# Optimization experiments

Measured on AMD Instinct MI355X. Metric: run time of the kernel, lower is better.

## Reference

```python
import jax, jax.numpy as jnp
import numpy as np

B, T, S, D, V = 32, 2048, 256, 1024, 56
STAR_PENALTY = -1.0
NEG = -1e30  # -inf surrogate that is safe for gradients


def setup_inputs() -> dict:
    key = jax.random.key(0)
    k1, k2, k3 = jax.random.split(key, 3)
    features = jax.random.normal(k1, (B, T, D), jnp.float32)
    targets = jax.random.randint(k2, (B, S), 1, V)  # 0 is the blank; labels in [1, V)
    W = jax.random.normal(k3, (V, D), jnp.float32) * (1.0 / 32.0)  # 1/sqrt(D)
    b = jnp.zeros((V,), jnp.float32)
    input_lengths = jnp.full((B,), T, jnp.int32)
    target_lengths = jnp.full((B,), S, jnp.int32)
    return dict(features=features, W=W, b=b, targets=targets,
                input_lengths=input_lengths, target_lengths=target_lengths)


def _star_ctc_losses(logp, targets, input_lengths, target_lengths, star_penalty):
    """Star-CTC forward (DP) score.
    logp: (T, N, C) log-softmax emissions; targets: (N, S) labels (blank=0 excluded).
    Extended state sequence [*, t1, *, t2, ..., tS, *]: star states play the role of
    CTC blanks but act as penalized wildcards, emitting logsumexp(logp)+star_penalty
    (== star_penalty for normalized log-probs). Standard CTC transition topology:
    self-loop, advance by 1, advance by 2 into a token state when it differs from the
    previous token. Returns per-sequence negative log-likelihood, shape (N,)."""
    Tlen, N, C = logp.shape
    Slen = targets.shape[1]
    L = 2 * Slen + 1
    ext = jnp.zeros((N, L), targets.dtype).at[:, 1::2].set(targets)  # (N, L)
    is_star = (jnp.arange(L) % 2 == 0)[None, :]                      # (1, L)
    prev2 = jnp.pad(ext[:, :-2], ((0, 0), (2, 0)), constant_values=-1)
    allow_skip = (~is_star) & (ext != prev2)                         # (N, L)

    def emit(logp_t):  # logp_t: (N, C) -> (N, L)
        star_e = star_penalty + jax.nn.logsumexp(logp_t, axis=-1, keepdims=True)
        tok_e = jnp.take_along_axis(logp_t, ext, axis=-1)
        return jnp.where(is_star, star_e, tok_e)

    alpha0 = jnp.where(jnp.arange(L)[None, :] < 2, emit(logp[0]), NEG)

    def step(alpha, xs):
        logp_t, t = xs
        a1 = jnp.pad(alpha[:, :-1], ((0, 0), (1, 0)), constant_values=NEG)
        a2 = jnp.where(allow_skip,
                       jnp.pad(alpha[:, :-2], ((0, 0), (2, 0)), constant_values=NEG),
                       NEG)
        new = jnp.logaddexp(jnp.logaddexp(alpha, a1), a2) + emit(logp_t)
        new = jnp.where(t < input_lengths[:, None], new, alpha)  # freeze past input_length
        return new, None

    alpha, _ = jax.lax.scan(step, alpha0, (logp[1:], jnp.arange(1, Tlen)))
    last = 2 * target_lengths                  # index of the final star state
    rows = jnp.arange(N)
    score = jnp.logaddexp(alpha[rows, last], alpha[rows, last - 1])
    return -score


def reference(features, W, b, targets, input_lengths, target_lengths):
    # classifier + log_softmax (Dropout(0.2) is identity at eval time)
    logits = jnp.einsum('btd,vd->btv', features, W) + b
    logp = jax.nn.log_softmax(logits.astype(jnp.float32), axis=-1)
    logp = jnp.transpose(logp, (1, 0, 2))      # (T, N, C) as in logits.permute(1,0,2)
    losses = _star_ctc_losses(logp, targets, input_lengths, target_lengths, STAR_PENALTY)
    # ctc_reduce_mean: length-normalized mean loss
    return jnp.mean(losses / target_lengths.astype(losses.dtype))
```

## Files before the change

### kernel.cpp

```cpp
#include <hip/hip_runtime.h>
#include <hip/hip_bf16.h>
#include <math.h>

typedef __attribute__((ext_vector_type(4))) float f32x4;
typedef __attribute__((ext_vector_type(8))) short s16x8;

#define LOG2E 1.4426950408889634f
#define LN2f  0.6931471805599453f
#define INV_E 0.36787944117144233f

__device__ __forceinline__ short bfc(float x) {
  unsigned u = __float_as_uint(x);
  unsigned r = u + 0x7fffu + ((u >> 16) & 1u);
  return (short)(r >> 16);
}

__device__ __forceinline__ unsigned pk2(float x, float y) {
  union { __hip_bfloat162 h; unsigned u; } c;
  c.h = __float22bfloat162_rn(make_float2(x, y));
  return c.u;
}

__device__ __forceinline__ float bperm(float v, int byte_addr) {
  return __int_as_float(__builtin_amdgcn_ds_bpermute(byte_addr, __float_as_int(v)));
}

__device__ __forceinline__ float rdlane(float v, int lane) {
  return __int_as_float(__builtin_amdgcn_readlane(__float_as_int(v), lane));
}

__global__ void conv_w(const float* __restrict__ W, short* __restrict__ Wb,
                       int V, int D) {
  int idx = blockIdx.x * blockDim.x + threadIdx.x;
  if (idx >= 64 * D) return;
  int row = idx / D, col = idx - row * D;
  Wb[idx] = (row < V) ? bfc(W[(size_t)row * D + col]) : (short)0;
}

__global__ __launch_bounds__(256) void gemm_pexp(
    const float* __restrict__ feat, const short* __restrict__ Wb,
    const float* __restrict__ bias, float* __restrict__ pt,
    int nrows, int D, int V) {
  const int lane = threadIdx.x & 63;
  const int wave = threadIdx.x >> 6;
  const int m_lo = lane & 15;
  const int q = lane >> 4;
  const int rowbase = (blockIdx.x * 4 + wave) * 32;

  int arow0 = rowbase + m_lo;
  int arow1 = rowbase + 16 + m_lo;
  if (arow0 >= nrows) arow0 = nrows - 1;
  if (arow1 >= nrows) arow1 = nrows - 1;
  const float* Ap0 = feat + (size_t)arow0 * D + q * 8;
  const float* Ap1 = feat + (size_t)arow1 * D + q * 8;
  const short* Bp = Wb + (size_t)m_lo * D + q * 8;
  const size_t bstr = (size_t)16 * D;

  f32x4 acc[2][4];
  #pragma unroll
  for (int g = 0; g < 2; ++g)
    #pragma unroll
    for (int ni = 0; ni < 4; ++ni) acc[g][ni] = (f32x4){0.f, 0.f, 0.f, 0.f};

  float4 al0 = *(const float4*)(Ap0);
  float4 ah0 = *(const float4*)(Ap0 + 4);
  float4 al1 = *(const float4*)(Ap1);
  float4 ah1 = *(const float4*)(Ap1 + 4);
  s16x8 b0 = *(const s16x8*)(Bp);
  s16x8 b1 = *(const s16x8*)(Bp + bstr);
  s16x8 b2 = *(const s16x8*)(Bp + 2 * bstr);
  s16x8 b3 = *(const s16x8*)(Bp + 3 * bstr);

  for (int k0 = 0; k0 < D; k0 += 32) {
    const int kn = (k0 + 32 < D) ? (k0 + 32) : 0;
    const float* Ap0n = feat + (size_t)arow0 * D + kn + q * 8;
    const float* Ap1n = feat + (size_t)arow1 * D + kn + q * 8;
    const short* Bpn = Wb + (size_t)m_lo * D + kn + q * 8;
    float4 nal0 = *(const float4*)(Ap0n);
    float4 nah0 = *(const float4*)(Ap0n + 4);
    float4 nal1 = *(const float4*)(Ap1n);
    float4 nah1 = *(const float4*)(Ap1n + 4);
    s16x8 nb0 = *(const s16x8*)(Bpn);
    s16x8 nb1 = *(const s16x8*)(Bpn + bstr);
    s16x8 nb2 = *(const s16x8*)(Bpn + 2 * bstr);
    s16x8 nb3 = *(const s16x8*)(Bpn + 3 * bstr);

    union { s16x8 v; unsigned u[4]; } av0, av1;
    av0.u[0] = pk2(al0.x, al0.y); av0.u[1] = pk2(al0.z, al0.w);
    av0.u[2] = pk2(ah0.x, ah0.y); av0.u[3] = pk2(ah0.z, ah0.w);
    av1.u[0] = pk2(al1.x, al1.y); av1.u[1] = pk2(al1.z, al1.w);
    av1.u[2] = pk2(ah1.x, ah1.y); av1.u[3] = pk2(ah1.z, ah1.w);

    acc[0][0] = __builtin_amdgcn_mfma_f32_16x16x32_bf16(av0.v, b0, acc[0][0], 0, 0, 0);
    acc[0][1] = __builtin_amdgcn_mfma_f32_16x16x32_bf16(av0.v, b1, acc[0][1], 0, 0, 0);
    acc[0][2] = __builtin_amdgcn_mfma_f32_16x16x32_bf16(av0.v, b2, acc[0][2], 0, 0, 0);
    acc[0][3] = __builtin_amdgcn_mfma_f32_16x16x32_bf16(av0.v, b3, acc[0][3], 0, 0, 0);
    acc[1][0] = __builtin_amdgcn_mfma_f32_16x16x32_bf16(av1.v, b0, acc[1][0], 0, 0, 0);
    acc[1][1] = __builtin_amdgcn_mfma_f32_16x16x32_bf16(av1.v, b1, acc[1][1], 0, 0, 0);
    acc[1][2] = __builtin_amdgcn_mfma_f32_16x16x32_bf16(av1.v, b2, acc[1][2], 0, 0, 0);
    acc[1][3] = __builtin_amdgcn_mfma_f32_16x16x32_bf16(av1.v, b3, acc[1][3], 0, 0, 0);

    al0 = nal0; ah0 = nah0; al1 = nal1; ah1 = nah1;
    b0 = nb0; b1 = nb1; b2 = nb2; b3 = nb3;
  }

  float bias_v[4];
  #pragma unroll
  for (int ni = 0; ni < 4; ++ni) {
    int col = ni * 16 + m_lo;
    bias_v[ni] = (col < V) ? bias[col] : 0.f;
  }

  #pragma unroll
  for (int g = 0; g < 2; ++g) {
    #pragma unroll
    for (int r = 0; r < 4; ++r) {
      int grow = rowbase + g * 16 + q * 4 + r;
      float lg[4];
      #pragma unroll
      for (int ni = 0; ni < 4; ++ni) {
        int col = ni * 16 + m_lo;
        lg[ni] = (col < V) ? (acc[g][ni][r] + bias_v[ni]) : -1e30f;
      }
      float m = fmaxf(fmaxf(lg[0], lg[1]), fmaxf(lg[2], lg[3]));
      #pragma unroll
      for (int off = 1; off < 16; off <<= 1) m = fmaxf(m, __shfl_xor(m, off));
      float p[4];
      #pragma unroll
      for (int ni = 0; ni < 4; ++ni) p[ni] = exp2f((lg[ni] - m) * LOG2E);
      float s = (p[0] + p[1]) + (p[2] + p[3]);
      #pragma unroll
      for (int off = 1; off < 16; off <<= 1) s += __shfl_xor(s, off);

      if (grow < nrows) {
        float* orow = pt + (size_t)grow * 64;
        orow[m_lo] = p[0];
        orow[16 + m_lo] = p[1];
        orow[32 + m_lo] = p[2];
        if (m_lo < 8)       orow[48 + m_lo] = p[3];
        else if (m_lo == 8) orow[56] = logf(s);
        else if (m_lo == 9) orow[57] = s * INV_E;
        else                orow[48 + m_lo] = 0.f;
      }
    }
  }
}

__global__ __launch_bounds__(64) void star_dp(
    const float* __restrict__ pt, const int* __restrict__ targets,
    const int* __restrict__ in_len, const int* __restrict__ tgt_len,
    float* __restrict__ partial, int T, int S) {
  const int n = blockIdx.x;
  const int lane = threadIdx.x;
  const float* row = pt + (size_t)n * T * 64;
  const int len = in_len[n];
  const int tl = tgt_len[n];
  const int* tg = targets + (size_t)n * S;

  const int s0 = lane * 4;
  int lab1 = (s0     < S) ? tg[s0]     : 0;
  int lab3 = (s0 + 1 < S) ? tg[s0 + 1] : 0;
  int lab5 = (s0 + 2 < S) ? tg[s0 + 2] : 0;
  int lab7 = (s0 + 3 < S) ? tg[s0 + 3] : 0;
  int labm1 = __shfl_up(lab7, 1);
  int labm3 = __shfl_up(lab5, 1);
  const bool sk1 = (lane > 0) && (lab1 != labm1);
  const bool sk3 = (lab3 != lab1);
  const bool sk5 = (lab5 != lab3);
  const bool sk7 = (lab7 != lab5);
  const bool skm1 = (labm1 != labm3);
  const int ad1 = lab1 << 2, ad3 = lab3 << 2, ad5 = lab5 << 2, ad7 = lab7 << 2;
  const int adm1 = labm1 << 2;

  float a0 = 0, a1 = 0, a2 = 0, a3 = 0, a4 = 0, a5 = 0, a6 = 0, a7 = 0, a8 = 0;
  float m1 = 0.f, m2 = 0.f, m3 = 0.f;
  int eps = 0, eL = 0;
  bool act = (lane == 0);

#define ROWL(t) row[(size_t)(((t) < len) ? (t) : (len - 1)) * 64 + lane]

  float rc = row[lane];
  {
    float star = rdlane(rc, 57);
    float e1i = bperm(rc, ad1);
    if (lane == 0) { a0 = star; a1 = e1i; }
  }
  float ksum = rc;

  float rr0 = ROWL(1), rr1 = ROWL(2), rr2 = ROWL(3), rr3 = ROWL(4);
  float rr4 = ROWL(5), rr5 = ROWL(6), rr6 = ROWL(7), rr7 = ROWL(8);

  float es0v = rdlane(rr0, 57);
  float e1a = bperm(rr0, ad1), e3a = bperm(rr0, ad3);
  float e5a = bperm(rr0, ad5), e7a = bperm(rr0, ad7);
  float em1a = bperm(rr0, adm1);
  float es1v = rdlane(rr1, 57);
  float e1b = bperm(rr1, ad1), e3b = bperm(rr1, ad3);
  float e5b = bperm(rr1, ad5), e7b = bperm(rr1, ad7);

#define RENORM()                                                             \
  do {                                                                       \
    float mx = fmaxf(fmaxf(fmaxf(a0, a1), fmaxf(a2, a3)),                    \
                     fmaxf(fmaxf(a4, a5), fmaxf(a6, a7)));                   \
    mx = fmaxf(mx, a8);                                                      \
    int e = (int)((__float_as_uint(mx) >> 23) & 255) - 126;                  \
    e = (act && mx > 0.f) ? e : 0;                                           \
    a0 = ldexpf(a0, -e); a1 = ldexpf(a1, -e); a2 = ldexpf(a2, -e);           \
    a3 = ldexpf(a3, -e); a4 = ldexpf(a4, -e); a5 = ldexpf(a5, -e);           \
    a6 = ldexpf(a6, -e); a7 = ldexpf(a7, -e); a8 = ldexpf(a8, -e);           \
    eps += e;                                                                \
  } while (0)

#define PAIR(C0, C1, N0, N1, P0, P1, DOREN)                                  \
  do {                                                                       \
    ksum += C0; ksum += C1;                                                  \
    if (!act) eps = eL;                                                      \
    bool inc = (lane != 0) &&                                                \
               ((m1 != 0.f) || (m2 != 0.f) || (m3 != 0.f));                  \
    int d = inc ? (eL - eps) : 0;                                            \
    if (__builtin_expect(d > 24, 0)) {                  \
      a0 = ldexpf(a0, -d); a1 = ldexpf(a1, -d); a2 = ldexpf(a2, -d);         \
      a3 = ldexpf(a3, -d); a4 = ldexpf(a4, -d); a5 = ldexpf(a5, -d);         \
      a6 = ldexpf(a6, -d); a7 = ldexpf(a7, -d); a8 = ldexpf(a8, -d);         \
      eps += d;                                      \
    } else {                                                                 \
      m1 = ldexpf(m1, d); m2 = ldexpf(m2, d); m3 = ldexpf(m3, d);            \
    }                                                                        \
    act = act || (m1 != 0.f) || (m2 != 0.f) || (m3 != 0.f);                  \
                  \
    a8 = (a8 + a7) * es0v;                                                   \
    a7 = (a7 + a6 + (sk7 ? a5 : 0.f)) * e7a;                                 \
    a6 = (a6 + a5) * es0v;                                                   \
    a5 = (a5 + a4 + (sk5 ? a3 : 0.f)) * e5a;                                 \
    a4 = (a4 + a3) * es0v;                                                   \
    a3 = (a3 + a2 + (sk3 ? a1 : 0.f)) * e3a;                                 \
    a2 = (a2 + a1) * es0v;                                                   \
    a1 = (a1 + a0 + (sk1 ? m1 : 0.f)) * e1a;                                 \
    a0 = (a0 + m1) * es0v;                                                   \
    m1 = (m1 + m2 + (skm1 ? m3 : 0.f)) * em1a;                               \
                                                             \
    a8 = (a8 + a7) * es1v;                                                   \
    a7 = (a7 + a6 + (sk7 ? a5 : 0.f)) * e7b;                                 \
    a6 = (a6 + a5) * es1v;                                                   \
    a5 = (a5 + a4 + (sk5 ? a3 : 0.f)) * e5b;                                 \
    a4 = (a4 + a3) * es1v;                                                   \
    a3 = (a3 + a2 + (sk3 ? a1 : 0.f)) * e3b;                                 \
    a2 = (a2 + a1) * es1v;                                                   \
    a1 = (a1 + a0 + (sk1 ? m1 : 0.f)) * e1b;                                 \
    a0 = (a0 + m1) * es1v;                                                   \
    C0 = ROWL(P0); C1 = ROWL(P1);                     \
    if (DOREN) RENORM();                                                     \
      \
    es0v = rdlane(N0, 57);                                                   \
    e1a = bperm(N0, ad1); e3a = bperm(N0, ad3);                              \
    e5a = bperm(N0, ad5); e7a = bperm(N0, ad7);                              \
    em1a = bperm(N0, adm1);                                                  \
    es1v = rdlane(N1, 57);                                                   \
    e1b = bperm(N1, ad1); e3b = bperm(N1, ad3);                              \
    e5b = bperm(N1, ad5); e7b = bperm(N1, ad7);                              \
                          \
    m3 = __shfl_up(a5, 1); m2 = __shfl_up(a6, 1); m1 = __shfl_up(a7, 1);     \
    eL = __shfl_up(eps, 1);                                                  \
    if (lane == 0) { m1 = 0.f; m2 = 0.f; m3 = 0.f; }                         \
  } while (0)

  int t0 = 1;
  for (; t0 + 8 <= len; t0 += 8) {
    PAIR(rr0, rr1, rr2, rr3, t0 + 8,  t0 + 9,  false);
    PAIR(rr2, rr3, rr4, rr5, t0 + 10, t0 + 11, false);
    PAIR(rr4, rr5, rr6, rr7, t0 + 12, t0 + 13, false);
    PAIR(rr6, rr7, rr0, rr1, t0 + 14, t0 + 15, true);
  }

  for (int t = t0; t < len; ++t) {
    float cur = ROWL(t);
    float esv = rdlane(cur, 57);
    float e1v = bperm(cur, ad1), e3v = bperm(cur, ad3);
    float e5v = bperm(cur, ad5), e7v = bperm(cur, ad7);
    ksum += cur;
    if (!act) eps = eL;
    bool inc = (lane != 0) && (m1 != 0.f);
    int d = inc ? (eL - eps) : 0;
    float m1s;
    if (__builtin_expect(d > 24, 0)) {
      a0 = ldexpf(a0, -d); a1 = ldexpf(a1, -d); a2 = ldexpf(a2, -d);
      a3 = ldexpf(a3, -d); a4 = ldexpf(a4, -d); a5 = ldexpf(a5, -d);
      a6 = ldexpf(a6, -d); a7 = ldexpf(a7, -d); a8 = ldexpf(a8, -d);
      eps += d; m1s = m1;
    } else {
      m1s = inc ? ldexpf(m1, d) : 0.f;
    }
    act = act || (m1s != 0.f);
    a8 = (a8 + a7) * esv;
    a7 = (a7 + a6 + (sk7 ? a5 : 0.f)) * e7v;
    a6 = (a6 + a5) * esv;
    a5 = (a5 + a4 + (sk5 ? a3 : 0.f)) * e5v;
    a4 = (a4 + a3) * esv;
    a3 = (a3 + a2 + (sk3 ? a1 : 0.f)) * e3v;
    a2 = (a2 + a1) * esv;
    a1 = (a1 + a0 + (sk1 ? m1s : 0.f)) * e1v;
    a0 = (a0 + m1s) * esv;
    if ((t & 7) == 0) RENORM();
    m1 = __shfl_up(a7, 1);
    eL = __shfl_up(eps, 1);
    if (lane == 0) m1 = 0.f;
  }

  __shared__ float sh[64 * 9];
  __shared__ int she[64];
  sh[lane * 9 + 0] = a0; sh[lane * 9 + 1] = a1; sh[lane * 9 + 2] = a2;
  sh[lane * 9 + 3] = a3; sh[lane * 9 + 4] = a4; sh[lane * 9 + 5] = a5;
  sh[lane * 9 + 6] = a6; sh[lane * 9 + 7] = a7; sh[lane * 9 + 8] = a8;
  she[lane] = eps;
  float k56 = __shfl(ksum, 56);
  __syncthreads();
  if (lane == 0) {
    int last = 2 * tl;
    int kx = last >> 3, jx = last & 7;
    if (kx > 63) { kx = 63; jx = last - 504; }
    int ky = (last - 1) >> 3, jy = (last - 1) & 7;
    float sx = sh[kx * 9 + jx]; int ex = she[kx];
    float sy = sh[ky * 9 + jy]; int ey = she[ky];
    int em = (ex > ey) ? ex : ey;
    float v = ldexpf(sx, ex - em) + ldexpf(sy, ey - em);
    float score = logf(v) + (float)em * LN2f - k56;
    partial[n] = -score / (float)tl;
  }
}

__global__ void reduce_mean(const float* __restrict__ partial,
                            float* __restrict__ out, int B) {
  float v = 0.f;
  for (int i = threadIdx.x; i < B; i += 64) v += partial[i];
  #pragma unroll
  for (int off = 32; off > 0; off >>= 1) v += __shfl_down(v, off, 64);
  if (threadIdx.x == 0) out[0] = v / (float)B;
}

extern "C" void kernel_launch(void* const* d_in, const int* in_sizes, int n_in,
                              void* d_out, int out_size, void* d_ws, size_t ws_size,
                              hipStream_t stream) {
  const float* feat = (const float*)d_in[0];
  const float* W = (const float*)d_in[1];
  const float* bias = (const float*)d_in[2];
  const int* targets = (const int*)d_in[3];
  const int* in_len = (const int*)d_in[4];
  const int* tgt_len = (const int*)d_in[5];
  float* out = (float*)d_out;

  const int V = in_sizes[2];
  const int D = in_sizes[1] / V;
  const int B = in_sizes[4];
  const int T = in_sizes[0] / (B * D);
  const int S = in_sizes[3] / B;
  const int nrows = B * T;

  float* pt = (float*)d_ws;
  float* partial = pt + (size_t)nrows * 64;
  short* Wb = (short*)(partial + B);

  conv_w<<<(64 * D + 255) / 256, 256, 0, stream>>>(W, Wb, V, D);

  dim3 g1((nrows + 127) / 128);
  gemm_pexp<<<g1, 256, 0, stream>>>(feat, Wb, bias, pt, nrows, D, V);

  star_dp<<<B, 64, 0, stream>>>(pt, targets, in_len, tgt_len, partial, T, S);

  reduce_mean<<<1, 64, 0, stream>>>(partial, out, B);
}
```

Measured before the change: 723.1 us.

## Fuse GEMM and star-CTC DP into one kernel with per-chunk ready flags

Merges the emission GEMM/softmax kernel and the sequential DP kernel into one launch. The first B blocks run the DP and spin on per-(batch, 128-timestep chunk) flags set with release atomics by GEMM blocks, so the DP can start before the whole GEMM finishes and the two phases overlap. The final state lookup also moves from shared memory to register selection plus shuffles. The cost is spin-waiting on flags, an extra memset, and a dependence on DP blocks being scheduled early. Since DP blocks have the lowest indices, GEMM blocks can still occupy the GPU alongside them.

Result: slower. 754.8 us (+4.4%).

```diff
diff --git a/kernel.cpp b/kernel.cpp
--- a/kernel.cpp
+++ b/kernel.cpp
@@ -27,6 +27,21 @@
 
 __device__ __forceinline__ float rdlane(float v, int lane) {
   return __int_as_float(__builtin_amdgcn_readlane(__float_as_int(v), lane));
+}
+
+__device__ __forceinline__ float pick9(int j, float a0, float a1, float a2,
+                                       float a3, float a4, float a5, float a6,
+                                       float a7, float a8) {
+  float v = a0;
+  if (j == 1) v = a1;
+  if (j == 2) v = a2;
+  if (j == 3) v = a3;
+  if (j == 4) v = a4;
+  if (j == 5) v = a5;
+  if (j == 6) v = a6;
+  if (j == 7) v = a7;
+  if (j == 8) v = a8;
+  return v;
 }
 
 __global__ void conv_w(const float* __restrict__ W, short* __restrict__ Wb,
@@ -37,125 +52,154 @@
   Wb[idx] = (row < V) ? bfc(W[(size_t)row * D + col]) : (short)0;
 }
 
-__global__ __launch_bounds__(256) void gemm_pexp(
+__global__ __launch_bounds__(256) void fused_gemm_star(
     const float* __restrict__ feat, const short* __restrict__ Wb,
     const float* __restrict__ bias, float* __restrict__ pt,
-    int nrows, int D, int V) {
-  const int lane = threadIdx.x & 63;
-  const int wave = threadIdx.x >> 6;
-  const int m_lo = lane & 15;
-  const int q = lane >> 4;
-  const int rowbase = (blockIdx.x * 4 + wave) * 32;
-
-  int arow0 = rowbase + m_lo;
-  int arow1 = rowbase + 16 + m_lo;
-  if (arow0 >= nrows) arow0 = nrows - 1;
-  if (arow1 >= nrows) arow1 = nrows - 1;
-  const float* Ap0 = feat + (size_t)arow0 * D + q * 8;
-  const float* Ap1 = feat + (size_t)arow1 * D + q * 8;
-  const short* Bp = Wb + (size_t)m_lo * D + q * 8;
-  const size_t bstr = (size_t)16 * D;
-
-  f32x4 acc[2][4];
-  #pragma unroll
-  for (int g = 0; g < 2; ++g)
+    int* __restrict__ flags,
+    const int* __restrict__ targets, const int* __restrict__ in_len,
+    const int* __restrict__ tgt_len, float* __restrict__ partial,
+    int nrows, int D, int V, int T, int S, int B, int CPB) {
+
+  if ((int)blockIdx.x >= B) {
+    const int j = blockIdx.x - B;
+    const int b = j % B;
+    const int c = j / B;
+    const int tc0 = c * 128;
+    const int rlen = (T - tc0 < 128) ? (T - tc0) : 128;
+    const int rowlim = b * T + tc0 + rlen;
+
+    const int lane = threadIdx.x & 63;
+    const int wave = threadIdx.x >> 6;
+    const int m_lo = lane & 15;
+    const int q = lane >> 4;
+    const int rowbase = b * T + tc0 + wave * 32;
+
+    int arow0 = rowbase + m_lo;
+    int arow1 = rowbase + 16 + m_lo;
+    if (arow0 >= nrows) arow0 = nrows - 1;
+    if (arow1 >= nrows) arow1 = nrows - 1;
+    const float* Ap0 = feat + (size_t)arow0 * D + q * 8;
+    const float* Ap1 = feat + (size_t)arow1 * D + q * 8;
+    const short* Bp = Wb + (size_t)m_lo * D + q * 8;
+    const size_t bstr = (size_t)16 * D;
+
+    f32x4 acc[2][4];
     #pragma unroll
-    for (int ni = 0; ni < 4; ++ni) acc[g][ni] = (f32x4){0.f, 0.f, 0.f, 0.f};
-
-  float4 al0 = *(const float4*)(Ap0);
-  float4 ah0 = *(const float4*)(Ap0 + 4);
-  float4 al1 = *(const float4*)(Ap1);
-  float4 ah1 = *(const float4*)(Ap1 + 4);
-  s16x8 b0 = *(const s16x8*)(Bp);
-  s16x8 b1 = *(const s16x8*)(Bp + bstr);
-  s16x8 b2 = *(const s16x8*)(Bp + 2 * bstr);
-  s16x8 b3 = *(const s16x8*)(Bp + 3 * bstr);
-
-  for (int k0 = 0; k0 < D; k0 += 32) {
-    const int kn = (k0 + 32 < D) ? (k0 + 32) : 0;
-    const float* Ap0n = feat + (size_t)arow0 * D + kn + q * 8;
-    const float* Ap1n = feat + (size_t)arow1 * D + kn + q * 8;
-    const short* Bpn = Wb + (size_t)m_lo * D + kn + q * 8;
-    float4 nal0 = *(const float4*)(Ap0n);
-    float4 nah0 = *(const float4*)(Ap0n + 4);
-    float4 nal1 = *(const float4*)(Ap1n);
-    float4 nah1 = *(const float4*)(Ap1n + 4);
-    s16x8 nb0 = *(const s16x8*)(Bpn);
-    s16x8 nb1 = *(const s16x8*)(Bpn + bstr);
-    s16x8 nb2 = *(const s16x8*)(Bpn + 2 * bstr);
-    s16x8 nb3 = *(const s16x8*)(Bpn + 3 * bstr);
-
-    union { s16x8 v; unsigned u[4]; } av0, av1;
-    av0.u[0] = pk2(al0.x, al0.y); av0.u[1] = pk2(al0.z, al0.w);
-    av0.u[2] = pk2(ah0.x, ah0.y); av0.u[3] = pk2(ah0.z, ah0.w);
-    av1.u[0] = pk2(al1.x, al1.y); av1.u[1] = pk2(al1.z, al1.w);
-    av1.u[2] = pk2(ah1.x, ah1.y); av1.u[3] = pk2(ah1.z, ah1.w);
-
-    acc[0][0] = __builtin_amdgcn_mfma_f32_16x16x32_bf16(av0.v, b0, acc[0][0], 0, 0, 0);
-    acc[0][1] = __builtin_amdgcn_mfma_f32_16x16x32_bf16(av0.v, b1, acc[0][1], 0, 0, 0);
-    acc[0][2] = __builtin_amdgcn_mfma_f32_16x16x32_bf16(av0.v, b2, acc[0][2], 0, 0, 0);
-    acc[0][3] = __builtin_amdgcn_mfma_f32_16x16x32_bf16(av0.v, b3, acc[0][3], 0, 0, 0);
-    acc[1][0] = __builtin_amdgcn_mfma_f32_16x16x32_bf16(av1.v, b0, acc[1][0], 0, 0, 0);
-    acc[1][1] = __builtin_amdgcn_mfma_f32_16x16x32_bf16(av1.v, b1, acc[1][1], 0, 0, 0);
-    acc[1][2] = __builtin_amdgcn_mfma_f32_16x16x32_bf16(av1.v, b2, acc[1][2], 0, 0, 0);
-    acc[1][3] = __builtin_amdgcn_mfma_f32_16x16x32_bf16(av1.v, b3, acc[1][3], 0, 0, 0);
-
-    al0 = nal0; ah0 = nah0; al1 = nal1; ah1 = nah1;
-    b0 = nb0; b1 = nb1; b2 = nb2; b3 = nb3;
-  }
-
-  float bias_v[4];
-  #pragma unroll
-  for (int ni = 0; ni < 4; ++ni) {
-    int col = ni * 16 + m_lo;
-    bias_v[ni] = (col < V) ? bias[col] : 0.f;
-  }
-
-  #pragma unroll
-  for (int g = 0; g < 2; ++g) {
+    for (int g = 0; g < 2; ++g)
+      #pragma unroll
+      for (int ni = 0; ni < 4; ++ni) acc[g][ni] = (f32x4){0.f, 0.f, 0.f, 0.f};
+
+    float4 al0 = *(const float4*)(Ap0);
+    float4 ah0 = *(const float4*)(Ap0 + 4);
+    float4 al1 = *(const float4*)(Ap1);
+    float4 ah1 = *(const float4*)(Ap1 + 4);
+    s16x8 b0 = *(const s16x8*)(Bp);
+    s16x8 b1 = *(const s16x8*)(Bp + bstr);
+    s16x8 b2 = *(const s16x8*)(Bp + 2 * bstr);
+    s16x8 b3 = *(const s16x8*)(Bp + 3 * bstr);
+
+    for (int k0 = 0; k0 < D; k0 += 32) {
+      const int kn = (k0 + 32 < D) ? (k0 + 32) : 0;
+      const float* Ap0n = feat + (size_t)arow0 * D + kn + q * 8;
+      const float* Ap1n = feat + (size_t)arow1 * D + kn + q * 8;
+      const short* Bpn = Wb + (size_t)m_lo * D + kn + q * 8;
+      float4 nal0 = *(const float4*)(Ap0n);
+      float4 nah0 = *(const float4*)(Ap0n + 4);
+      float4 nal1 = *(const float4*)(Ap1n);
+      float4 nah1 = *(const float4*)(Ap1n + 4);
+      s16x8 nb0 = *(const s16x8*)(Bpn);
+      s16x8 nb1 = *(const s16x8*)(Bpn + bstr);
+      s16x8 nb2 = *(const s16x8*)(Bpn + 2 * bstr);
+      s16x8 nb3 = *(const s16x8*)(Bpn + 3 * bstr);
+
+      union { s16x8 v; unsigned u[4]; } av0, av1;
+      av0.u[0] = pk2(al0.x, al0.y); av0.u[1] = pk2(al0.z, al0.w);
+      av0.u[2] = pk2(ah0.x, ah0.y); av0.u[3] = pk2(ah0.z, ah0.w);
+      av1.u[0] = pk2(al1.x, al1.y); av1.u[1] = pk2(al1.z, al1.w);
+      av1.u[2] = pk2(ah1.x, ah1.y); av1.u[3] = pk2(ah1.z, ah1.w);
+
+      acc[0][0] = __builtin_amdgcn_mfma_f32_16x16x32_bf16(av0.v, b0, acc[0][0], 0, 0, 0);
+      acc[0][1] = __builtin_amdgcn_mfma_f32_16x16x32_bf16(av0.v, b1, acc[0][1], 0, 0, 0);
+      acc[0][2] = __builtin_amdgcn_mfma_f32_16x16x32_bf16(av0.v, b2, acc[0][2], 0, 0, 0);
+      acc[0][3] = __builtin_amdgcn_mfma_f32_16x16x32_bf16(av0.v, b3, acc[0][3], 0, 0, 0);
+      acc[1][0] = __builtin_amdgcn_mfma_f32_16x16x32_bf16(av1.v, b0, acc[1][0], 0, 0, 0);
+      acc[1][1] = __builtin_amdgcn_mfma_f32_16x16x32_bf16(av1.v, b1, acc[1][1], 0, 0, 0);
+      acc[1][2] = __builtin_amdgcn_mfma_f32_16x16x32_bf16(av1.v, b2, acc[1][2], 0, 0, 0);
+      acc[1][3] = __builtin_amdgcn_mfma_f32_16x16x32_bf16(av1.v, b3, acc[1][3], 0, 0, 0);
+
+      al0 = nal0; ah0 = nah0; al1 = nal1; ah1 = nah1;
+      b0 = nb0; b1 = nb1; b2 = nb2; b3 = nb3;
+    }
+
+    float bias_v[4];
     #pragma unroll
-    for (int r = 0; r < 4; ++r) {
-      int grow = rowbase + g * 16 + q * 4 + r;
-      float lg[4];
+    for (int ni = 0; ni < 4; ++ni) {
+      int col = ni * 16 + m_lo;
+      bias_v[ni] = (col < V) ? bias[col] : 0.f;
+    }
+
+    #pragma unroll
+    for (int g = 0; g < 2; ++g) {
       #pragma unroll
-      for (int ni = 0; ni < 4; ++ni) {
-        int col = ni * 16 + m_lo;
-        lg[ni] = (col < V) ? (acc[g][ni][r] + bias_v[ni]) : -1e30f;
-      }
-      float m = fmaxf(fmaxf(lg[0], lg[1]), fmaxf(lg[2], lg[3]));
-      #pragma unroll
-      for (int off = 1; off < 16; off <<= 1) m = fmaxf(m, __shfl_xor(m, off));
-      float p[4];
-      #pragma unroll
-      for (int ni = 0; ni < 4; ++ni) p[ni] = exp2f((lg[ni] - m) * LOG2E);
-      float s = (p[0] + p[1]) + (p[2] + p[3]);
-      #pragma unroll
-      for (int off = 1; off < 16; off <<= 1) s += __shfl_xor(s, off);
-
-      if (grow < nrows) {
-        float* orow = pt + (size_t)grow * 64;
-        orow[m_lo] = p[0];
-        orow[16 + m_lo] = p[1];
-        orow[32 + m_lo] = p[2];
-        if (m_lo < 8)       orow[48 + m_lo] = p[3];
-        else if (m_lo == 8) orow[56] = logf(s);
-        else if (m_lo == 9) orow[57] = s * INV_E;
-        else                orow[48 + m_lo] = 0.f;
+      for (int r = 0; r < 4; ++r) {
+        int grow = rowbase + g * 16 + q * 4 + r;
+        float lg[4];
+        #pragma unroll
+        for (int ni = 0; ni < 4; ++ni) {
+          int col = ni * 16 + m_lo;
+          lg[ni] = (col < V) ? (acc[g][ni][r] + bias_v[ni]) : -1e30f;
+        }
+        float m = fmaxf(fmaxf(lg[0], lg[1]), fmaxf(lg[2], lg[3]));
+        #pragma unroll
+        for (int off = 1; off < 16; off <<= 1) m = fmaxf(m, __shfl_xor(m, off));
+        float p[4];
+        #pragma unroll
+        for (int ni = 0; ni < 4; ++ni) p[ni] = exp2f((lg[ni] - m) * LOG2E);
+        float s = (p[0] + p[1]) + (p[2] + p[3]);
+        #pragma unroll
+        for (int off = 1; off < 16; off <<= 1) s += __shfl_xor(s, off);
+
+        if (grow < rowlim) {
+          float* orow = pt + (size_t)grow * 64;
+          orow[m_lo] = p[0];
+          orow[16 + m_lo] = p[1];
+          orow[32 + m_lo] = p[2];
+          if (m_lo < 8)       orow[48 + m_lo] = p[3];
+          else if (m_lo == 8) orow[56] = logf(s);
+          else if (m_lo == 9) orow[57] = s * INV_E;
+          else                orow[48 + m_lo] = 0.f;
+        }
       }
     }
+
+    __syncthreads();
+    if (threadIdx.x == 0)
+      __hip_atomic_store(&flags[b * CPB + c], 1, __ATOMIC_RELEASE,
+                         __HIP_MEMORY_SCOPE_AGENT);
+    return;
   }
-}
-
-__global__ __launch_bounds__(64) void star_dp(
-    const float* __restrict__ pt, const int* __restrict__ targets,
-    const int* __restrict__ in_len, const int* __restrict__ tgt_len,
-    float* __restrict__ partial, int T, int S) {
+
+  if (threadIdx.x >= 64) return;
   const int n = blockIdx.x;
   const int lane = threadIdx.x;
   const float* row = pt + (size_t)n * T * 64;
   const int len = in_len[n];
   const int tl = tgt_len[n];
   const int* tg = targets + (size_t)n * S;
+  const int* fl = flags + n * CPB;
+
+  int cdone = -1;
+#define WAITC(cc)                                                            \
+  do {                                                                       \
+    int _c = (cc);                                                           \
+    while (cdone < _c) {                                                     \
+      if (__hip_atomic_load((int*)&fl[cdone + 1], __ATOMIC_ACQUIRE,          \
+                            __HIP_MEMORY_SCOPE_AGENT))                       \
+        ++cdone;                                                             \
+      else                                                                   \
+        __builtin_amdgcn_s_sleep(2);                                         \
+    }                                                                        \
+  } while (0)
 
   const int s0 = lane * 4;
   int lab1 = (s0     < S) ? tg[s0]     : 0;
@@ -178,6 +222,8 @@
   bool act = (lane == 0);
 
 #define ROWL(t) row[(size_t)(((t) < len) ? (t) : (len - 1)) * 64 + lane]
+
+  WAITC(0);
 
   float rc = row[lane];
   {
@@ -266,11 +312,16 @@
 
   int t0 = 1;
   for (; t0 + 8 <= len; t0 += 8) {
+    int tmax = t0 + 15;
+    if (tmax > len - 1) tmax = len - 1;
+    WAITC(tmax >> 7);
     PAIR(rr0, rr1, rr2, rr3, t0 + 8,  t0 + 9,  false);
     PAIR(rr2, rr3, rr4, rr5, t0 + 10, t0 + 11, false);
     PAIR(rr4, rr5, rr6, rr7, t0 + 12, t0 + 13, false);
     PAIR(rr6, rr7, rr0, rr1, t0 + 14, t0 + 15, true);
   }
+
+  WAITC((len - 1) >> 7);
 
   for (int t = t0; t < len; ++t) {
     float cur = ROWL(t);
@@ -306,26 +357,25 @@
     if (lane == 0) m1 = 0.f;
   }
 
-  __shared__ float sh[64 * 9];
-  __shared__ int she[64];
-  sh[lane * 9 + 0] = a0; sh[lane * 9 + 1] = a1; sh[lane * 9 + 2] = a2;
-  sh[lane * 9 + 3] = a3; sh[lane * 9 + 4] = a4; sh[lane * 9 + 5] = a5;
-  sh[lane * 9 + 6] = a6; sh[lane * 9 + 7] = a7; sh[lane * 9 + 8] = a8;
-  she[lane] = eps;
+  int last = 2 * tl;
+  int kx = last >> 3, jx = last & 7;
+  if (kx > 63) { kx = 63; jx = last - 504; }
+  int ky = (last - 1) >> 3, jy = (last - 1) & 7;
+  float vx = pick9(jx, a0, a1, a2, a3, a4, a5, a6, a7, a8);
+  float vy = pick9(jy, a0, a1, a2, a3, a4, a5, a6, a7, a8);
   float k56 = __shfl(ksum, 56);
-  __syncthreads();
+  float sx = __shfl(vx, kx); int ex = __shfl(eps, kx);
+  float sy = __shfl(vy, ky); int ey = __shfl(eps, ky);
   if (lane == 0) {
-    int last = 2 * tl;
-    int kx = last >> 3, jx = last & 7;
-    if (kx > 63) { kx = 63; jx = last - 504; }
-    int ky = (last - 1) >> 3, jy = (last - 1) & 7;
-    float sx = sh[kx * 9 + jx]; int ex = she[kx];
-    float sy = sh[ky * 9 + jy]; int ey = she[ky];
     int em = (ex > ey) ? ex : ey;
     float v = ldexpf(sx, ex - em) + ldexpf(sy, ey - em);
     float score = logf(v) + (float)em * LN2f - k56;
     partial[n] = -score / (float)tl;
   }
+#undef WAITC
+#undef ROWL
+#undef RENORM
+#undef PAIR
 }
 
 __global__ void reduce_mean(const float* __restrict__ partial,
@@ -358,13 +408,16 @@
   float* pt = (float*)d_ws;
   float* partial = pt + (size_t)nrows * 64;
   short* Wb = (short*)(partial + B);
+  const int CPB = (T + 127) / 128;
+  int* flags = (int*)((char*)Wb + (size_t)64 * D * sizeof(short));
+
+  hipMemsetAsync(flags, 0, (size_t)B * CPB * sizeof(int), stream);
 
   conv_w<<<(64 * D + 255) / 256, 256, 0, stream>>>(W, Wb, V, D);
 
-  dim3 g1((nrows + 127) / 128);
-  gemm_pexp<<<g1, 256, 0, stream>>>(feat, Wb, bias, pt, nrows, D, V);
-
-  star_dp<<<B, 64, 0, stream>>>(pt, targets, in_len, tgt_len, partial, T, S);
+  fused_gemm_star<<<dim3(B + B * CPB), 256, 0, stream>>>(
+      feat, Wb, bias, pt, flags, targets, in_len, tgt_len, partial,
+      nrows, D, V, T, S, B, CPB);
 
   reduce_mean<<<1, 64, 0, stream>>>(partial, out, B);
 }
```
